# Performance work log

Measured on AMD Instinct MI355X. Metric: run time of the kernel, lower is better.

Reference implementation:

```python
import jax, jax.numpy as jnp
import numpy as np

U, I, N, E, F, H, TOPK = 2048, 16384, 18432, 1_000_000, 64, 32, 3
NEG = -1e30  # stands in for 'structural zero' entries excluded from top-k


def setup_inputs() -> dict:
    key = jax.random.key(0)
    ks = jax.random.split(key, 6)
    x = jax.random.normal(ks[0], (N, F), dtype=jnp.float32)
    w1 = jax.random.normal(ks[1], (H, 2 * F + 2), dtype=jnp.float32) * 0.1
    b1 = jnp.zeros((H,), dtype=jnp.float32)
    w2 = jax.random.normal(ks[2], (1, H), dtype=jnp.float32) * 0.1
    b2 = jnp.zeros((1,), dtype=jnp.float32)
    edge_src = jax.random.randint(ks[3], (E,), 0, U)        # user-local == global (user_idx = arange)
    edge_dst_item = jax.random.randint(ks[4], (E,), 0, I)   # item-local; global item id = U + item
    user_idx = jnp.arange(U, dtype=jnp.int64) if jax.config.jax_enable_x64 else jnp.arange(U, dtype=jnp.int32)
    return {"x": x, "w1": w1, "b1": b1, "w2": w2, "b2": b2,
            "edge_src": edge_src, "edge_dst_item": edge_dst_item,
            "user_idx": user_idx, "num_nodes": N}


def reference(x, w1, b1, w2, b2, edge_src, edge_dst_item, user_idx, num_nodes):
    num_users = user_idx.shape[0]
    num_items = num_nodes - num_users
    u_local = edge_src           # user_idx = arange(U) so user_map is identity
    i_local = edge_dst_item      # item nodes occupy indices [U, N)

    ones = jnp.ones(u_local.shape[0], dtype=jnp.float32)
    d_u = jnp.log1p(jax.ops.segment_sum(ones, u_local, num_segments=num_users))  # [U]
    d_i = jnp.log1p(jax.ops.segment_sum(ones, i_local, num_segments=num_items))  # [I]

    # per-edge features: [u_x, log1p(deg_u), i_x, log1p(deg_i)] -> [E, 2F+2]
    x_u = x[user_idx[u_local]]
    x_it = x[num_users + i_local]
    x_e = jnp.concatenate([x_u, d_u[u_local][:, None], x_it, d_i[i_local][:, None]], axis=1)
    h = jax.nn.relu(x_e @ w1.T + b1)
    w = jax.nn.sigmoid(h @ w2.T + b2)[:, 0]  # [E], edge weights in (0,1)

    # A' [U, I] (duplicate edges coalesce-summed), C = A' A'^T with degree scaling
    A = jnp.zeros((num_users, num_items), dtype=jnp.float32).at[u_local, i_local].add(w)
    C = A @ A.T
    Dh = jnp.sqrt(d_u)
    C = C * Dh[:, None] * Dh[None, :]

    # per-row top-k restricted to structural nonzeros (all weights > 0)
    Cm = jnp.where(C > 0, C, NEG)
    vals, idx = jax.lax.top_k(Cm, TOPK)          # [U, K]
    valid = vals > 0
    vhalf = jnp.where(valid, vals, 0.0) * 0.5
    rows = jnp.broadcast_to(jnp.arange(num_users)[:, None], (num_users, TOPK))
    T = jnp.zeros((num_users, num_users), dtype=jnp.float32).at[rows, idx].add(vhalf)
    S = T + T.T  # symmetrized, deduped-by-sum adjacency; S[r,c] = val of edge (r,c)
    return S, d_u
```

## Files before the change

### kernel.cpp

```cpp
#include <hip/hip_runtime.h>
#include <hip/hip_bf16.h>
#include <math.h>

#define U_N 2048
#define I_N 16384
#define F_N 64
#define H_N 32
#define KDIM 16384
#define NEGV (-1e30f)
#define NB_DEG 256

typedef __attribute__((ext_vector_type(8))) short short8;
typedef __attribute__((ext_vector_type(4))) float f32x4;

__device__ __forceinline__ unsigned short f2bf(float f) {
    unsigned int u = __builtin_bit_cast(unsigned int, f);
    return (unsigned short)((u + 0x7fffu + ((u >> 16) & 1u)) >> 16);
}

__device__ __forceinline__ void gload16(const void* g, void* l) {
    __builtin_amdgcn_global_load_lds(
        (const __attribute__((address_space(1))) unsigned int*)g,
        (__attribute__((address_space(3))) unsigned int*)l, 16, 0, 0);
}

__global__ __launch_bounds__(256) void k_deg_part(const int* __restrict__ src,
                                                  const int* __restrict__ dst, int E,
                                                  unsigned int* __restrict__ pu,
                                                  unsigned int* __restrict__ pi2,
                                                  float* __restrict__ C,
                                                  float* __restrict__ out) {
    __shared__ unsigned int hu[U_N];
    __shared__ unsigned int hi2[I_N / 2];
    int tid = threadIdx.x;
    for (int t = tid; t < U_N; t += 256) hu[t] = 0u;
    for (int t = tid; t < I_N / 2; t += 256) hi2[t] = 0u;
    __syncthreads();
    const int4* s4 = (const int4*)src;
    const int4* d4 = (const int4*)dst;
    int nv = E >> 2;
    for (int v = blockIdx.x * 256 + tid; v < nv; v += NB_DEG * 256) {
        int4 u = s4[v], i = d4[v];
        atomicAdd(&hu[u.x], 1u); atomicAdd(&hi2[i.x >> 1], 1u << ((i.x & 1) * 16));
        atomicAdd(&hu[u.y], 1u); atomicAdd(&hi2[i.y >> 1], 1u << ((i.y & 1) * 16));
        atomicAdd(&hu[u.z], 1u); atomicAdd(&hi2[i.z >> 1], 1u << ((i.z & 1) * 16));
        atomicAdd(&hu[u.w], 1u); atomicAdd(&hi2[i.w >> 1], 1u << ((i.w & 1) * 16));
    }
    if (blockIdx.x == 0) {
        int e = nv * 4 + tid;
        if (e < E) {
            atomicAdd(&hu[src[e]], 1u);
            int i = dst[e];
            atomicAdd(&hi2[i >> 1], 1u << ((i & 1) * 16));
        }
    }
    __syncthreads();
    unsigned int* pub = pu + (size_t)blockIdx.x * U_N;
    unsigned int* pib = pi2 + (size_t)blockIdx.x * (I_N / 2);
    for (int t = tid; t < U_N; t += 256) pub[t] = hu[t];
    for (int t = tid; t < I_N / 2; t += 256) pib[t] = hi2[t];
    const float4 z4 = {0.f, 0.f, 0.f, 0.f};
    float4* C4 = (float4*)C;
    for (int t = blockIdx.x * 256 + tid; t < U_N * U_N / 4; t += NB_DEG * 256)
        C4[t] = z4;
    float4* o4 = (float4*)out;
    for (int t = blockIdx.x * 256 + tid; t < (U_N * U_N + U_N) / 4; t += NB_DEG * 256)
        o4[t] = z4;
}

__global__ __launch_bounds__(256) void k_node2(const unsigned int* __restrict__ pu,
                                               const unsigned int* __restrict__ pi2,
                                               float* __restrict__ du,
                                               float* __restrict__ di,
                                               float* __restrict__ Dh,
                                               float* __restrict__ out_du,
                                               unsigned int* __restrict__ degu) {
    __shared__ unsigned int red[8][32];
    int j = threadIdx.x >> 5, l = threadIdx.x & 31;
    int e = blockIdx.x * 32 + l;
    unsigned int s = 0;
    if (e < U_N) {
        const unsigned int* p = pu + e;
#pragma unroll
        for (int k = 0; k < 32; ++k) s += p[(size_t)(j * 32 + k) * U_N];
    } else {
        const unsigned int* p = pi2 + (e - U_N);
#pragma unroll
        for (int k = 0; k < 32; ++k) s += p[(size_t)(j * 32 + k) * (I_N / 2)];
    }
    red[j][l] = s;
    __syncthreads();
    if (threadIdx.x < 32) {
        unsigned int t = 0;
#pragma unroll
        for (int jj = 0; jj < 8; ++jj) t += red[jj][l];
        if (e < U_N) {
            degu[e] = t;
            float v = log1pf((float)t);
            du[e] = v;
            Dh[e] = sqrtf(v);
            out_du[e] = v;
        } else {
            int ii = e - U_N;
            di[2 * ii]     = log1pf((float)(t & 0xffffu));
            di[2 * ii + 1] = log1pf((float)(t >> 16));
        }
    }
}

__global__ __launch_bounds__(256) void k_pof(const unsigned int* __restrict__ pu,
                                             const unsigned int* __restrict__ degu,
                                             unsigned int* __restrict__ base,
                                             unsigned int* __restrict__ pof) {
    __shared__ unsigned int dg[U_N];
    __shared__ unsigned int wt[4];
    __shared__ unsigned int ps[8][32];
    int tid = threadIdx.x;
    int wave = tid >> 6, lane = tid & 63;
    for (int t = tid; t < U_N; t += 256) dg[t] = degu[t];
    __syncthreads();
    unsigned int loc[8];
    unsigned int s = 0;
#pragma unroll
    for (int j = 0; j < 8; ++j) { loc[j] = dg[tid * 8 + j]; s += loc[j]; }
    unsigned int inc = s;
#pragma unroll
    for (int off = 1; off < 64; off <<= 1) {
        unsigned int o = __shfl_up(inc, off);
        if (lane >= off) inc += o;
    }
    if (lane == 63) wt[wave] = inc;
    __syncthreads();
    unsigned int woff = 0;
#pragma unroll
    for (int w = 0; w < 4; ++w) woff += (w < wave) ? wt[w] : 0u;
    unsigned int ex = woff + inc - s;
    __syncthreads();
    {
        unsigned int run = ex;
#pragma unroll
        for (int j = 0; j < 8; ++j) { unsigned int v = loc[j]; dg[tid * 8 + j] = run; run += v; }
    }
    __syncthreads();
    int c = tid >> 5, l = tid & 31;
    int u = blockIdx.x * 32 + l;
    if (c == 0) base[u] = dg[u];
    unsigned int v32[32];
    unsigned int sum = 0;
#pragma unroll
    for (int k = 0; k < 32; ++k) {
        v32[k] = pu[(size_t)(c * 32 + k) * U_N + u];
        sum += v32[k];
    }
    ps[c][l] = sum;
    __syncthreads();
    unsigned int run = dg[u];
#pragma unroll
    for (int c2 = 0; c2 < 8; ++c2) run += (c2 < c) ? ps[c2][l] : 0u;
#pragma unroll
    for (int k = 0; k < 32; ++k) {
        pof[(size_t)(c * 32 + k) * U_N + u] = run;
        run += v32[k];
    }
}

__global__ __launch_bounds__(256) void k_esort(const int* __restrict__ src,
                                               const int* __restrict__ dst, int E,
                                               const unsigned int* __restrict__ pof,
                                               unsigned short* __restrict__ sorted) {
    __shared__ unsigned int cur[U_N];
    int tid = threadIdx.x;
    const unsigned int* p = pof + (size_t)blockIdx.x * U_N;
    for (int t = tid; t < U_N; t += 256) cur[t] = p[t];
    __syncthreads();
    const int4* s4 = (const int4*)src;
    const int4* d4 = (const int4*)dst;
    int nv = E >> 2;
    for (int v = blockIdx.x * 256 + tid; v < nv; v += NB_DEG * 256) {
        int4 u = s4[v], i = d4[v];
        sorted[atomicAdd(&cur[u.x], 1u)] = (unsigned short)i.x;
        sorted[atomicAdd(&cur[u.y], 1u)] = (unsigned short)i.y;
        sorted[atomicAdd(&cur[u.z], 1u)] = (unsigned short)i.z;
        sorted[atomicAdd(&cur[u.w], 1u)] = (unsigned short)i.w;
    }
    if (blockIdx.x == 0) {
        int e = nv * 4 + tid;
        if (e < E)
            sorted[atomicAdd(&cur[src[e]], 1u)] = (unsigned short)dst[e];
    }
}

__global__ __launch_bounds__(256) void k_proj(const float* __restrict__ x,
                                              const float* __restrict__ w1,
                                              const float* __restrict__ b1,
                                              const float* __restrict__ du,
                                              const float* __restrict__ di,
                                              float* __restrict__ Pu,
                                              float* __restrict__ Pi) {
    int t = blockIdx.x * 256 + threadIdx.x;
    if (t < U_N * H_N) {
        int u = t >> 5, j = t & 31;
        const float* xr = x + (size_t)u * F_N;
        const float* wr = w1 + (size_t)j * (2 * F_N + 2);
        float acc = b1[j] + du[u] * wr[64];
#pragma unroll
        for (int f = 0; f < F_N; ++f) acc = fmaf(xr[f], wr[f], acc);
        Pu[t] = acc;
    } else if (t < U_N * H_N + I_N * H_N) {
        int t2 = t - U_N * H_N;
        int i = t2 >> 5, j = t2 & 31;
        const float* xr = x + (size_t)(U_N + i) * F_N;
        const float* wr = w1 + (size_t)j * (2 * F_N + 2) + 65;
        float acc = di[i] * wr[64];
#pragma unroll
        for (int f = 0; f < F_N; ++f) acc = fmaf(xr[f], wr[f], acc);
        Pi[t2] = acc;
    }
}

__global__ __launch_bounds__(256) void k_edge2(const unsigned short* __restrict__ sorted,
                                               const unsigned int* __restrict__ base,
                                               const unsigned int* __restrict__ degu,
                                               const float* __restrict__ Pu,
                                               const float* __restrict__ Pi,
                                               const float* __restrict__ w2,
                                               const float* __restrict__ b2,
                                               uint4* __restrict__ Aw,
                                               float* __restrict__ diag) {
    __shared__ float hrow[I_N];
    __shared__ float red[256];
    int u = blockIdx.x, tid = threadIdx.x;
    float4* h4 = (float4*)hrow;
    float4 z4 = {0.f, 0.f, 0.f, 0.f};
#pragma unroll
    for (int j = 0; j < 16; ++j) h4[tid + j * 256] = z4;

    float pur[H_N], w2r[H_N];
#pragma unroll
    for (int j = 0; j < H_N; ++j) pur[j] = Pu[(size_t)u * H_N + j];
#pragma unroll
    for (int j = 0; j < H_N; ++j) w2r[j] = w2[j];
    float bb = b2[0];
    __syncthreads();

    int nb = (int)base[u], d = (int)degu[u];
    for (int k = tid; k < d; k += 256) {
        int i = (int)sorted[nb + k];
        const float4* pi4 = (const float4*)(Pi + (size_t)i * H_N);
        float acc = bb;
#pragma unroll
        for (int q = 0; q < H_N / 4; ++q) {
            float4 b = pi4[q];
            acc = fmaf(fmaxf(pur[4 * q + 0] + b.x, 0.f), w2r[4 * q + 0], acc);
            acc = fmaf(fmaxf(pur[4 * q + 1] + b.y, 0.f), w2r[4 * q + 1], acc);
            acc = fmaf(fmaxf(pur[4 * q + 2] + b.z, 0.f), w2r[4 * q + 2], acc);
            acc = fmaf(fmaxf(pur[4 * q + 3] + b.w, 0.f), w2r[4 * q + 3], acc);
        }
        float wgt = 1.0f / (1.0f + expf(-acc));
        atomicAdd(&hrow[i], wgt);
    }
    __syncthreads();

    uint4* row = Aw + (size_t)u * (I_N / 8);
    float ss = 0.f;
#pragma unroll
    for (int j = 0; j < 8; ++j) {
        int w = tid + j * 256;
        float4 a = h4[2 * w], b = h4[2 * w + 1];
        uint4 o;
        o.x = (unsigned int)f2bf(a.x) | ((unsigned int)f2bf(a.y) << 16);
        o.y = (unsigned int)f2bf(a.z) | ((unsigned int)f2bf(a.w) << 16);
        o.z = (unsigned int)f2bf(b.x) | ((unsigned int)f2bf(b.y) << 16);
        o.w = (unsigned int)f2bf(b.z) | ((unsigned int)f2bf(b.w) << 16);
        row[w] = o;
        ss = fmaf(a.x, a.x, ss); ss = fmaf(a.y, a.y, ss);
        ss = fmaf(a.z, a.z, ss); ss = fmaf(a.w, a.w, ss);
        ss = fmaf(b.x, b.x, ss); ss = fmaf(b.y, b.y, ss);
        ss = fmaf(b.z, b.z, ss); ss = fmaf(b.w, b.w, ss);
    }
    red[tid] = ss;
    __syncthreads();
#pragma unroll
    for (int s = 128; s > 0; s >>= 1) {
        if (tid < s) red[tid] += red[tid + s];
        __syncthreads();
    }
    if (tid == 0) diag[u] = red[0];
}

#define BM 128
#define BKS 64
#define NBLK (U_N / BM)
#define NPAIR (NBLK * (NBLK + 1) / 2)
#define KSPLIT 4
#define KCH (KDIM / KSPLIT)

__global__ __launch_bounds__(256) void k_syrk(const unsigned short* __restrict__ Abf,
                                              float* __restrict__ C) {
    __shared__ unsigned short As[BM * BKS];
    __shared__ unsigned short Bs[BM * BKS];

    int k0 = blockIdx.x * KCH;
    int p = blockIdx.y;
    int bi = 0, rem = p;
    while (rem >= NBLK - bi) { rem -= NBLK - bi; ++bi; }
    int bj = bi + rem;
    int diagp = (bi == bj);

    int tid = threadIdx.x;
    int wave = tid >> 6, lane = tid & 63;

    int srow = wave * 32 + (lane >> 3);
    int scol = ((lane & 7) ^ (lane >> 3)) * 8;
    const unsigned short* Ag = Abf + (size_t)(bi * BM + srow) * KDIM + k0 + scol;
    const unsigned short* Bg = Abf + (size_t)(bj * BM + srow) * KDIM + k0 + scol;
    unsigned short* lA = As + (wave * 32) * BKS;
    unsigned short* lB = Bs + (wave * 32) * BKS;

    int wm = wave >> 1, wn = wave & 1;
    int lm = lane & 15, lq = lane >> 4;
    int lm7 = lm & 7;
    const unsigned short* bTile = diagp ? As : Bs;

    f32x4 acc[4][4];
#pragma unroll
    for (int m = 0; m < 4; ++m)
#pragma unroll
        for (int n = 0; n < 4; ++n) acc[m][n] = (f32x4){0.f, 0.f, 0.f, 0.f};

    for (int kt = 0; kt < KCH; kt += BKS) {
        __syncthreads();
#pragma unroll
        for (int j = 0; j < 4; ++j)
            gload16(Ag + kt + (size_t)(j * 8) * KDIM, lA + j * 8 * BKS);
        if (!diagp) {
#pragma unroll
            for (int j = 0; j < 4; ++j)
                gload16(Bg + kt + (size_t)(j * 8) * KDIM, lB + j * 8 * BKS);
        }
        __syncthreads();

#pragma unroll
        for (int s = 0; s < 2; ++s) {
            int pos = ((lq + s * 4) ^ lm7) * 8;
            short8 av[4], bv[4];
#pragma unroll
            for (int m = 0; m < 4; ++m)
                av[m] = *(const short8*)(As + (wm * 64 + m * 16 + lm) * BKS + pos);
#pragma unroll
            for (int n = 0; n < 4; ++n)
                bv[n] = *(const short8*)(bTile + (wn * 64 + n * 16 + lm) * BKS + pos);
#pragma unroll
            for (int m = 0; m < 4; ++m)
#pragma unroll
                for (int n = 0; n < 4; ++n)
                    acc[m][n] = __builtin_amdgcn_mfma_f32_16x16x32_bf16(
                        av[m], bv[n], acc[m][n], 0, 0, 0);
        }
    }

#pragma unroll
    for (int m = 0; m < 4; ++m) {
        int rb = bi * BM + wm * 64 + m * 16 + lq * 4;
#pragma unroll
        for (int n = 0; n < 4; ++n) {
            int c = bj * BM + wn * 64 + n * 16 + lm;
            f32x4 v = acc[m][n];
#pragma unroll
            for (int g = 0; g < 4; ++g)
                atomicAdd(&C[(size_t)(rb + g) * U_N + c], v[g]);
        }
    }
}

__global__ __launch_bounds__(256) void k_mirror(float* __restrict__ C) {
    __shared__ float T[64][65];
    int tr = blockIdx.x, tc = blockIdx.y;
    if ((tr >> 1) <= (tc >> 1)) return;
    int lane = threadIdx.x & 63;
    int w = threadIdx.x >> 6;
#pragma unroll
    for (int s = 0; s < 16; ++s) {
        int r = s * 4 + w;
        T[r][lane] = C[(size_t)(tc * 64 + r) * U_N + tr * 64 + lane];
    }
    __syncthreads();
#pragma unroll
    for (int s = 0; s < 16; ++s) {
        int r = s * 4 + w;
        C[(size_t)(tr * 64 + r) * U_N + tc * 64 + lane] = T[lane][r];
    }
}

__device__ __forceinline__ bool better(float va, int ia, float vb, int ib) {
    return (va > vb) || (va == vb && ia < ib);
}
__device__ __forceinline__ void ins3(float v, int i, float& v0, int& i0,
                                     float& v1, int& i1, float& v2, int& i2) {
    if (better(v, i, v0, i0)) { v2 = v1; i2 = i1; v1 = v0; i1 = i0; v0 = v; i0 = i; }
    else if (better(v, i, v1, i1)) { v2 = v1; i2 = i1; v1 = v; i1 = i; }
    else if (better(v, i, v2, i2)) { v2 = v; i2 = i; }
}

__global__ __launch_bounds__(256) void k_topk(const float* __restrict__ C,
                                              const float* __restrict__ Dh,
                                              const float* __restrict__ diag,
                                              float* __restrict__ out) {
    int wave = threadIdx.x >> 6, lane = threadIdx.x & 63;
    int r = blockIdx.x * 4 + wave;
    float dr = Dh[r];
    float dex = diag[r] * dr * dr;
    float dval = (dex > 0.f) ? dex : NEGV;
    const float4* row = (const float4*)(C + (size_t)r * U_N);
    const float4* dh4 = (const float4*)Dh;
    float v0 = NEGV, v1 = NEGV, v2 = NEGV;
    int i0 = 0x7fffffff, i1 = 0x7fffffff, i2 = 0x7fffffff;
    int qr = r >> 2;
    for (int q = lane; q < U_N / 4; q += 64) {
        float4 cv = row[q];
        float4 dv = dh4[q];
        int c = q * 4;
        float x0 = (cv.x > 0.f) ? cv.x * dr * dv.x : NEGV;
        float x1 = (cv.y > 0.f) ? cv.y * dr * dv.y : NEGV;
        float x2 = (cv.z > 0.f) ? cv.z * dr * dv.z : NEGV;
        float x3 = (cv.w > 0.f) ? cv.w * dr * dv.w : NEGV;
        if (q == qr) {
            int j = r & 3;
            if (j == 0) x0 = dval; else if (j == 1) x1 = dval;
            else if (j == 2) x2 = dval; else x3 = dval;
        }
        if (better(x0, c + 0, v2, i2)) ins3(x0, c + 0, v0, i0, v1, i1, v2, i2);
        if (better(x1, c + 1, v2, i2)) ins3(x1, c + 1, v0, i0, v1, i1, v2, i2);
        if (better(x2, c + 2, v2, i2)) ins3(x2, c + 2, v0, i0, v1, i1, v2, i2);
        if (better(x3, c + 3, v2, i2)) ins3(x3, c + 3, v0, i0, v1, i1, v2, i2);
    }
#pragma unroll
    for (int off = 1; off < 64; off <<= 1) {
        float ov0 = __shfl_xor(v0, off), ov1 = __shfl_xor(v1, off), ov2 = __shfl_xor(v2, off);
        int oi0 = __shfl_xor(i0, off), oi1 = __shfl_xor(i1, off), oi2 = __shfl_xor(i2, off);
        ins3(ov0, oi0, v0, i0, v1, i1, v2, i2);
        ins3(ov1, oi1, v0, i0, v1, i1, v2, i2);
        ins3(ov2, oi2, v0, i0, v1, i1, v2, i2);
    }
    if (lane == 0) {
        float vs[3] = {v0, v1, v2};
        int is[3] = {i0, i1, i2};
#pragma unroll
        for (int k = 0; k < 3; ++k) {
            if (vs[k] > 0.f) {
                atomicAdd(&out[(size_t)r * U_N + is[k]], 0.5f * vs[k]);
                atomicAdd(&out[(size_t)is[k] * U_N + r], 0.5f * vs[k]);
            }
        }
    }
}

extern "C" void kernel_launch(void* const* d_in, const int* in_sizes, int n_in,
                              void* d_out, int out_size, void* d_ws, size_t ws_size,
                              hipStream_t stream) {
    const float* x  = (const float*)d_in[0];
    const float* w1 = (const float*)d_in[1];
    const float* b1 = (const float*)d_in[2];
    const float* w2 = (const float*)d_in[3];
    const float* b2 = (const float*)d_in[4];
    const int* esrc = (const int*)d_in[5];
    const int* edst = (const int*)d_in[6];
    int E = in_sizes[5];
    float* out = (float*)d_out;

    unsigned short* Abf = (unsigned short*)d_ws;
    float* C    = (float*)(Abf + (size_t)U_N * I_N);
    float* Pu   = C + (size_t)U_N * U_N;
    float* Pi   = Pu + (size_t)U_N * H_N;
    unsigned int* pu  = (unsigned int*)(Pi + (size_t)I_N * H_N);
    unsigned int* pi2 = pu + (size_t)NB_DEG * U_N;
    unsigned int* pof = pi2 + (size_t)NB_DEG * (I_N / 2);
    unsigned int* degu = pof + (size_t)NB_DEG * U_N;
    unsigned int* base = degu + U_N;
    float* du   = (float*)(base + U_N);
    float* di   = du + U_N;
    float* Dh   = di + I_N;
    float* diag = Dh + U_N;
    unsigned short* sorted = (unsigned short*)(diag + U_N);

    k_deg_part<<<NB_DEG, 256, 0, stream>>>(esrc, edst, E, pu, pi2, C, out);
    k_node2<<<(U_N + I_N / 2) / 32, 256, 0, stream>>>(pu, pi2, du, di, Dh,
                                                      out + (size_t)U_N * U_N, degu);
    k_pof<<<U_N / 32, 256, 0, stream>>>(pu, degu, base, pof);
    k_proj<<<(U_N * H_N + I_N * H_N) / 256, 256, 0, stream>>>(x, w1, b1, du, di, Pu, Pi);
    k_esort<<<NB_DEG, 256, 0, stream>>>(esrc, edst, E, pof, sorted);
    k_edge2<<<U_N, 256, 0, stream>>>(sorted, base, degu, Pu, Pi, w2, b2,
                                     (uint4*)Abf, diag);
    k_syrk<<<dim3(KSPLIT, NPAIR), 256, 0, stream>>>(Abf, C);
    k_mirror<<<dim3(U_N / 64, U_N / 64), 256, 0, stream>>>(C);
    k_topk<<<U_N / 4, 256, 0, stream>>>(C, Dh, diag, out);
}
```

Measured before the change: 299.9 us.

## Double-buffer SYRK LDS tiles, fuse esort with projection, widen blocks to 1024

The SYRK kernel now keeps two LDS buffers per operand, so the next K-slice is loaded while MFMAs run on the current one, with a single barrier per iteration. The edge sort and the node projection are merged into one launch whose blocks branch by block index, removing one kernel launch and letting both run concurrently. The degree, sort and edge kernels move from 256 to 1024 threads per block, and the per-row diagonal reduction uses wave shuffles instead of a shared-memory tree. Risks include occupancy loss from 1024-thread blocks holding large LDS arrays, and the single barrier per iteration may not fully protect the buffer being overwritten if the async LDS loads are not waited on.

New measurement: 315.0 us. +5.0%, slower.

```diff
diff --git a/kernel.cpp b/kernel.cpp
--- a/kernel.cpp
+++ b/kernel.cpp
@@ -24,22 +24,22 @@
         (__attribute__((address_space(3))) unsigned int*)l, 16, 0, 0);
 }
 
-__global__ __launch_bounds__(256) void k_deg_part(const int* __restrict__ src,
-                                                  const int* __restrict__ dst, int E,
-                                                  unsigned int* __restrict__ pu,
-                                                  unsigned int* __restrict__ pi2,
-                                                  float* __restrict__ C,
-                                                  float* __restrict__ out) {
+__global__ __launch_bounds__(1024) void k_deg_part(const int* __restrict__ src,
+                                                   const int* __restrict__ dst, int E,
+                                                   unsigned int* __restrict__ pu,
+                                                   unsigned int* __restrict__ pi2,
+                                                   float* __restrict__ C,
+                                                   float* __restrict__ out) {
     __shared__ unsigned int hu[U_N];
     __shared__ unsigned int hi2[I_N / 2];
     int tid = threadIdx.x;
-    for (int t = tid; t < U_N; t += 256) hu[t] = 0u;
-    for (int t = tid; t < I_N / 2; t += 256) hi2[t] = 0u;
+    for (int t = tid; t < U_N; t += 1024) hu[t] = 0u;
+    for (int t = tid; t < I_N / 2; t += 1024) hi2[t] = 0u;
     __syncthreads();
     const int4* s4 = (const int4*)src;
     const int4* d4 = (const int4*)dst;
     int nv = E >> 2;
-    for (int v = blockIdx.x * 256 + tid; v < nv; v += NB_DEG * 256) {
+    for (int v = blockIdx.x * 1024 + tid; v < nv; v += NB_DEG * 1024) {
         int4 u = s4[v], i = d4[v];
         atomicAdd(&hu[u.x], 1u); atomicAdd(&hi2[i.x >> 1], 1u << ((i.x & 1) * 16));
         atomicAdd(&hu[u.y], 1u); atomicAdd(&hi2[i.y >> 1], 1u << ((i.y & 1) * 16));
@@ -57,14 +57,14 @@
     __syncthreads();
     unsigned int* pub = pu + (size_t)blockIdx.x * U_N;
     unsigned int* pib = pi2 + (size_t)blockIdx.x * (I_N / 2);
-    for (int t = tid; t < U_N; t += 256) pub[t] = hu[t];
-    for (int t = tid; t < I_N / 2; t += 256) pib[t] = hi2[t];
+    for (int t = tid; t < U_N; t += 1024) pub[t] = hu[t];
+    for (int t = tid; t < I_N / 2; t += 1024) pib[t] = hi2[t];
     const float4 z4 = {0.f, 0.f, 0.f, 0.f};
     float4* C4 = (float4*)C;
-    for (int t = blockIdx.x * 256 + tid; t < U_N * U_N / 4; t += NB_DEG * 256)
+    for (int t = blockIdx.x * 1024 + tid; t < U_N * U_N / 4; t += NB_DEG * 1024)
         C4[t] = z4;
     float4* o4 = (float4*)out;
-    for (int t = blockIdx.x * 256 + tid; t < (U_N * U_N + U_N) / 4; t += NB_DEG * 256)
+    for (int t = blockIdx.x * 1024 + tid; t < (U_N * U_N + U_N) / 4; t += NB_DEG * 1024)
         o4[t] = z4;
 }
 
@@ -164,76 +164,80 @@
     }
 }
 
-__global__ __launch_bounds__(256) void k_esort(const int* __restrict__ src,
-                                               const int* __restrict__ dst, int E,
-                                               const unsigned int* __restrict__ pof,
-                                               unsigned short* __restrict__ sorted) {
+#define NPROJ (((U_N + I_N) * H_N) / 1024)
+__global__ __launch_bounds__(1024) void k_pe(const int* __restrict__ src,
+                                             const int* __restrict__ dst, int E,
+                                             const unsigned int* __restrict__ pof,
+                                             unsigned short* __restrict__ sorted,
+                                             const float* __restrict__ x,
+                                             const float* __restrict__ w1,
+                                             const float* __restrict__ b1,
+                                             const float* __restrict__ du,
+                                             const float* __restrict__ di,
+                                             float* __restrict__ Pu,
+                                             float* __restrict__ Pi) {
     __shared__ unsigned int cur[U_N];
     int tid = threadIdx.x;
-    const unsigned int* p = pof + (size_t)blockIdx.x * U_N;
-    for (int t = tid; t < U_N; t += 256) cur[t] = p[t];
-    __syncthreads();
-    const int4* s4 = (const int4*)src;
-    const int4* d4 = (const int4*)dst;
-    int nv = E >> 2;
-    for (int v = blockIdx.x * 256 + tid; v < nv; v += NB_DEG * 256) {
-        int4 u = s4[v], i = d4[v];
-        sorted[atomicAdd(&cur[u.x], 1u)] = (unsigned short)i.x;
-        sorted[atomicAdd(&cur[u.y], 1u)] = (unsigned short)i.y;
-        sorted[atomicAdd(&cur[u.z], 1u)] = (unsigned short)i.z;
-        sorted[atomicAdd(&cur[u.w], 1u)] = (unsigned short)i.w;
-    }
-    if (blockIdx.x == 0) {
-        int e = nv * 4 + tid;
-        if (e < E)
-            sorted[atomicAdd(&cur[src[e]], 1u)] = (unsigned short)dst[e];
-    }
-}
-
-__global__ __launch_bounds__(256) void k_proj(const float* __restrict__ x,
-                                              const float* __restrict__ w1,
-                                              const float* __restrict__ b1,
-                                              const float* __restrict__ du,
-                                              const float* __restrict__ di,
-                                              float* __restrict__ Pu,
-                                              float* __restrict__ Pi) {
-    int t = blockIdx.x * 256 + threadIdx.x;
-    if (t < U_N * H_N) {
-        int u = t >> 5, j = t & 31;
-        const float* xr = x + (size_t)u * F_N;
-        const float* wr = w1 + (size_t)j * (2 * F_N + 2);
-        float acc = b1[j] + du[u] * wr[64];
-#pragma unroll
-        for (int f = 0; f < F_N; ++f) acc = fmaf(xr[f], wr[f], acc);
-        Pu[t] = acc;
-    } else if (t < U_N * H_N + I_N * H_N) {
-        int t2 = t - U_N * H_N;
-        int i = t2 >> 5, j = t2 & 31;
-        const float* xr = x + (size_t)(U_N + i) * F_N;
-        const float* wr = w1 + (size_t)j * (2 * F_N + 2) + 65;
-        float acc = di[i] * wr[64];
-#pragma unroll
-        for (int f = 0; f < F_N; ++f) acc = fmaf(xr[f], wr[f], acc);
-        Pi[t2] = acc;
-    }
-}
-
-__global__ __launch_bounds__(256) void k_edge2(const unsigned short* __restrict__ sorted,
-                                               const unsigned int* __restrict__ base,
-                                               const unsigned int* __restrict__ degu,
-                                               const float* __restrict__ Pu,
-                                               const float* __restrict__ Pi,
-                                               const float* __restrict__ w2,
-                                               const float* __restrict__ b2,
-                                               uint4* __restrict__ Aw,
-                                               float* __restrict__ diag) {
+    int bid = blockIdx.x;
+    if (bid < NB_DEG) {
+        const unsigned int* p = pof + (size_t)bid * U_N;
+        for (int t = tid; t < U_N; t += 1024) cur[t] = p[t];
+        __syncthreads();
+        const int4* s4 = (const int4*)src;
+        const int4* d4 = (const int4*)dst;
+        int nv = E >> 2;
+        for (int v = bid * 1024 + tid; v < nv; v += NB_DEG * 1024) {
+            int4 u = s4[v], i = d4[v];
+            sorted[atomicAdd(&cur[u.x], 1u)] = (unsigned short)i.x;
+            sorted[atomicAdd(&cur[u.y], 1u)] = (unsigned short)i.y;
+            sorted[atomicAdd(&cur[u.z], 1u)] = (unsigned short)i.z;
+            sorted[atomicAdd(&cur[u.w], 1u)] = (unsigned short)i.w;
+        }
+        if (bid == 0) {
+            int e = nv * 4 + tid;
+            if (e < E)
+                sorted[atomicAdd(&cur[src[e]], 1u)] = (unsigned short)dst[e];
+        }
+    } else {
+        int t = (bid - NB_DEG) * 1024 + tid;
+        if (t < U_N * H_N) {
+            int u = t >> 5, j = t & 31;
+            const float* xr = x + (size_t)u * F_N;
+            const float* wr = w1 + (size_t)j * (2 * F_N + 2);
+            float acc = b1[j] + du[u] * wr[64];
+#pragma unroll
+            for (int f = 0; f < F_N; ++f) acc = fmaf(xr[f], wr[f], acc);
+            Pu[t] = acc;
+        } else {
+            int t2 = t - U_N * H_N;
+            int i = t2 >> 5, j = t2 & 31;
+            const float* xr = x + (size_t)(U_N + i) * F_N;
+            const float* wr = w1 + (size_t)j * (2 * F_N + 2) + 65;
+            float acc = di[i] * wr[64];
+#pragma unroll
+            for (int f = 0; f < F_N; ++f) acc = fmaf(xr[f], wr[f], acc);
+            Pi[t2] = acc;
+        }
+    }
+}
+
+__global__ __launch_bounds__(1024) void k_edge2(const unsigned short* __restrict__ sorted,
+                                                const unsigned int* __restrict__ base,
+                                                const unsigned int* __restrict__ degu,
+                                                const float* __restrict__ Pu,
+                                                const float* __restrict__ Pi,
+                                                const float* __restrict__ w2,
+                                                const float* __restrict__ b2,
+                                                uint4* __restrict__ Aw,
+                                                float* __restrict__ diag) {
     __shared__ float hrow[I_N];
-    __shared__ float red[256];
+    __shared__ float red[16];
     int u = blockIdx.x, tid = threadIdx.x;
+    int wave = tid >> 6, lane = tid & 63;
     float4* h4 = (float4*)hrow;
     float4 z4 = {0.f, 0.f, 0.f, 0.f};
 #pragma unroll
-    for (int j = 0; j < 16; ++j) h4[tid + j * 256] = z4;
+    for (int j = 0; j < 4; ++j) h4[tid + j * 1024] = z4;
 
     float pur[H_N], w2r[H_N];
 #pragma unroll
@@ -244,7 +248,7 @@
     __syncthreads();
 
     int nb = (int)base[u], d = (int)degu[u];
-    for (int k = tid; k < d; k += 256) {
+    for (int k = tid; k < d; k += 1024) {
         int i = (int)sorted[nb + k];
         const float4* pi4 = (const float4*)(Pi + (size_t)i * H_N);
         float acc = bb;
@@ -264,8 +268,8 @@
     uint4* row = Aw + (size_t)u * (I_N / 8);
     float ss = 0.f;
 #pragma unroll
-    for (int j = 0; j < 8; ++j) {
-        int w = tid + j * 256;
+    for (int j = 0; j < 2; ++j) {
+        int w = tid + j * 1024;
         float4 a = h4[2 * w], b = h4[2 * w + 1];
         uint4 o;
         o.x = (unsigned int)f2bf(a.x) | ((unsigned int)f2bf(a.y) << 16);
@@ -278,14 +282,16 @@
         ss = fmaf(b.x, b.x, ss); ss = fmaf(b.y, b.y, ss);
         ss = fmaf(b.z, b.z, ss); ss = fmaf(b.w, b.w, ss);
     }
-    red[tid] = ss;
-    __syncthreads();
-#pragma unroll
-    for (int s = 128; s > 0; s >>= 1) {
-        if (tid < s) red[tid] += red[tid + s];
-        __syncthreads();
-    }
-    if (tid == 0) diag[u] = red[0];
+#pragma unroll
+    for (int off = 32; off > 0; off >>= 1) ss += __shfl_down(ss, off);
+    if (lane == 0) red[wave] = ss;
+    __syncthreads();
+    if (tid == 0) {
+        float t = 0.f;
+#pragma unroll
+        for (int w = 0; w < 16; ++w) t += red[w];
+        diag[u] = t;
+    }
 }
 
 #define BM 128
@@ -297,8 +303,8 @@
 
 __global__ __launch_bounds__(256) void k_syrk(const unsigned short* __restrict__ Abf,
                                               float* __restrict__ C) {
-    __shared__ unsigned short As[BM * BKS];
-    __shared__ unsigned short Bs[BM * BKS];
+    __shared__ unsigned short As[2][BM * BKS];
+    __shared__ unsigned short Bs[2][BM * BKS];
 
     int k0 = blockIdx.x * KCH;
     int p = blockIdx.y;
@@ -314,13 +320,14 @@
     int scol = ((lane & 7) ^ (lane >> 3)) * 8;
     const unsigned short* Ag = Abf + (size_t)(bi * BM + srow) * KDIM + k0 + scol;
     const unsigned short* Bg = Abf + (size_t)(bj * BM + srow) * KDIM + k0 + scol;
-    unsigned short* lA = As + (wave * 32) * BKS;
-    unsigned short* lB = Bs + (wave * 32) * BKS;
+    unsigned short* lA0 = &As[0][(wave * 32) * BKS];
+    unsigned short* lA1 = &As[1][(wave * 32) * BKS];
+    unsigned short* lB0 = &Bs[0][(wave * 32) * BKS];
+    unsigned short* lB1 = &Bs[1][(wave * 32) * BKS];
 
     int wm = wave >> 1, wn = wave & 1;
     int lm = lane & 15, lq = lane >> 4;
     int lm7 = lm & 7;
-    const unsigned short* bTile = diagp ? As : Bs;
 
     f32x4 acc[4][4];
 #pragma unroll
@@ -328,28 +335,42 @@
 #pragma unroll
         for (int n = 0; n < 4; ++n) acc[m][n] = (f32x4){0.f, 0.f, 0.f, 0.f};
 
+#pragma unroll
+    for (int j = 0; j < 4; ++j)
+        gload16(Ag + (size_t)(j * 8) * KDIM, lA0 + j * 8 * BKS);
+    if (!diagp) {
+#pragma unroll
+        for (int j = 0; j < 4; ++j)
+            gload16(Bg + (size_t)(j * 8) * KDIM, lB0 + j * 8 * BKS);
+    }
+    __syncthreads();
+
     for (int kt = 0; kt < KCH; kt += BKS) {
-        __syncthreads();
-#pragma unroll
-        for (int j = 0; j < 4; ++j)
-            gload16(Ag + kt + (size_t)(j * 8) * KDIM, lA + j * 8 * BKS);
-        if (!diagp) {
+        int cur = (kt >> 6) & 1;
+        if (kt + BKS < KCH) {
+            unsigned short* sA = cur ? lA0 : lA1;
+            unsigned short* sB = cur ? lB0 : lB1;
 #pragma unroll
             for (int j = 0; j < 4; ++j)
-                gload16(Bg + kt + (size_t)(j * 8) * KDIM, lB + j * 8 * BKS);
-        }
-        __syncthreads();
-
+                gload16(Ag + kt + BKS + (size_t)(j * 8) * KDIM, sA + j * 8 * BKS);
+            if (!diagp) {
+#pragma unroll
+                for (int j = 0; j < 4; ++j)
+                    gload16(Bg + kt + BKS + (size_t)(j * 8) * KDIM, sB + j * 8 * BKS);
+            }
+        }
+        const unsigned short* aT = &As[cur][0];
+        const unsigned short* bT = diagp ? aT : &Bs[cur][0];
 #pragma unroll
         for (int s = 0; s < 2; ++s) {
             int pos = ((lq + s * 4) ^ lm7) * 8;
             short8 av[4], bv[4];
 #pragma unroll
             for (int m = 0; m < 4; ++m)
-                av[m] = *(const short8*)(As + (wm * 64 + m * 16 + lm) * BKS + pos);
+                av[m] = *(const short8*)(aT + (wm * 64 + m * 16 + lm) * BKS + pos);
 #pragma unroll
             for (int n = 0; n < 4; ++n)
-                bv[n] = *(const short8*)(bTile + (wn * 64 + n * 16 + lm) * BKS + pos);
+                bv[n] = *(const short8*)(bT + (wn * 64 + n * 16 + lm) * BKS + pos);
 #pragma unroll
             for (int m = 0; m < 4; ++m)
 #pragma unroll
@@ -357,6 +378,7 @@
                     acc[m][n] = __builtin_amdgcn_mfma_f32_16x16x32_bf16(
                         av[m], bv[n], acc[m][n], 0, 0, 0);
         }
+        __syncthreads();
     }
 
 #pragma unroll
@@ -483,14 +505,14 @@
     float* diag = Dh + U_N;
     unsigned short* sorted = (unsigned short*)(diag + U_N);
 
-    k_deg_part<<<NB_DEG, 256, 0, stream>>>(esrc, edst, E, pu, pi2, C, out);
+    k_deg_part<<<NB_DEG, 1024, 0, stream>>>(esrc, edst, E, pu, pi2, C, out);
     k_node2<<<(U_N + I_N / 2) / 32, 256, 0, stream>>>(pu, pi2, du, di, Dh,
                                                       out + (size_t)U_N * U_N, degu);
     k_pof<<<U_N / 32, 256, 0, stream>>>(pu, degu, base, pof);
-    k_proj<<<(U_N * H_N + I_N * H_N) / 256, 256, 0, stream>>>(x, w1, b1, du, di, Pu, Pi);
-    k_esort<<<NB_DEG, 256, 0, stream>>>(esrc, edst, E, pof, sorted);
-    k_edge2<<<U_N, 256, 0, stream>>>(sorted, base, degu, Pu, Pi, w2, b2,
-                                     (uint4*)Abf, diag);
+    k_pe<<<NB_DEG + NPROJ, 1024, 0, stream>>>(esrc, edst, E, pof, sorted,
+                                              x, w1, b1, du, di, Pu, Pi);
+    k_edge2<<<U_N, 1024, 0, stream>>>(sorted, base, degu, Pu, Pi, w2, b2,
+                                      (uint4*)Abf, diag);
     k_syrk<<<dim3(KSPLIT, NPAIR), 256, 0, stream>>>(Abf, C);
     k_mirror<<<dim3(U_N / 64, U_N / 64), 256, 0, stream>>>(C);
     k_topk<<<U_N / 4, 256, 0, stream>>>(C, Dh, diag, out);
```
